# Performance work log

Hardware: AMD Instinct MI355X
Metric: run time of the kernel (lower is better)

The kernel has to match this reference:

```python
import jax, jax.numpy as jnp
import numpy as np

N, NFEAT, NHID, NREL, NCLASS, NHEADS = 4096, 512, 64, 64, 16, 8
ALPHA = 0.2   # LeakyReLU negative slope
NEG = -9e15   # pyGAT mask value


def _gat_layer(x, rel, mask, adj_ad, W, a1, a2, concat):
    # x: [N, Fin], rel: [nrel, Fin], mask: [N, N] bool, adj_ad: [N, nrel]
    xr = x + adj_ad @ rel                 # relation-augmented node features
    h = xr @ W                            # [N, Fout]
    f1 = h @ a1                           # [N]  (a^T[Wh_i||Wh_j] = f1_i + f2_j)
    f2 = h @ a2                           # [N]
    e = jax.nn.leaky_relu(f1[:, None] + f2[None, :], ALPHA)  # [N, N]
    att = jax.nn.softmax(jnp.where(mask, e, NEG), axis=1)
    out = att @ h                         # [N, Fout]
    return jax.nn.elu(out) if concat else out


def setup_inputs() -> dict:
    key = jax.random.key(0)
    ks = jax.random.split(key, 12)
    x = jax.random.normal(ks[0], (N, NFEAT), jnp.float32)
    rel = jax.random.normal(ks[1], (NREL, NFEAT), jnp.float32)
    rel_dict = jax.random.randint(ks[2], (N,), 0, NREL, jnp.int32)
    adj = (jax.random.uniform(ks[3], (N, N)) < 0.01).astype(jnp.float32)
    adj = jnp.maximum(adj, jnp.eye(N, dtype=jnp.float32))  # self loops
    adj_ad = jax.random.uniform(ks[4], (N, NREL), jnp.float32)
    adj_ad = adj_ad / adj_ad.sum(axis=1, keepdims=True)
    s_in = 1.0 / np.sqrt(NFEAT)
    s_hid = 1.0 / np.sqrt(NHID)
    s_cat = 1.0 / np.sqrt(NHID * NHEADS)
    W_heads = jax.random.normal(ks[5], (NHEADS, NFEAT, NHID), jnp.float32) * s_in
    a1_heads = jax.random.normal(ks[6], (NHEADS, NHID), jnp.float32) * s_hid
    a2_heads = jax.random.normal(ks[7], (NHEADS, NHID), jnp.float32) * s_hid
    W_out = jax.random.normal(ks[8], (NHID * NHEADS, NFEAT), jnp.float32) * s_cat
    a1_out = jax.random.normal(ks[9], (NFEAT,), jnp.float32) * s_in
    a2_out = jax.random.normal(ks[10], (NFEAT,), jnp.float32) * s_in
    lin_W = jax.random.normal(ks[11], (NFEAT, NCLASS), jnp.float32) * s_in
    lin_b = jnp.zeros((NCLASS,), jnp.float32)
    return {"x": x, "rel": rel, "rel_dict": rel_dict, "adj": adj, "adj_ad": adj_ad,
            "W_heads": W_heads, "a1_heads": a1_heads, "a2_heads": a2_heads,
            "W_out": W_out, "a1_out": a1_out, "a2_out": a2_out,
            "lin_W": lin_W, "lin_b": lin_b}


def reference(x, rel, rel_dict, adj, adj_ad, W_heads, a1_heads, a2_heads,
              W_out, a1_out, a2_out, lin_W, lin_b):
    # dropout is identity at inference (training=False); rel_dict is only used
    # by the repo to build adj/adj_ad, so it is a non-math constant here.
    mask = adj > 0
    # multi-head GAT layer, heads fused via vmap then concatenated on feature dim
    heads = jax.vmap(lambda W, a1, a2: _gat_layer(x, rel, mask, adj_ad, W, a1, a2, True))(
        W_heads, a1_heads, a2_heads)                      # [H, N, NHID]
    hcat = jnp.moveaxis(heads, 0, 1).reshape(N, NHEADS * NHID)  # [N, H*NHID]
    h2 = _gat_layer(hcat, rel, mask, adj_ad, W_out, a1_out, a2_out, False)  # [N, NFEAT]
    logits = jax.nn.elu(h2 @ lin_W + lin_b)               # [N, NCLASS]
    return jax.nn.log_softmax(logits, axis=1)
```

## Files before the change

kernel.cpp:

```cpp
#include <hip/hip_runtime.h>

#define NN      4096
#define FEAT    512
#define NHID    64
#define NHEADS  8
#define NCLS    16
#define MAXDEG  128
#define ALPHA   0.2f

typedef __bf16 bf16_t;
typedef __bf16 bf16x8_t __attribute__((ext_vector_type(8)));
typedef float  f32x4_t  __attribute__((ext_vector_type(4)));
typedef unsigned short us8_t __attribute__((ext_vector_type(8)));

__device__ inline unsigned short f2bf(float f) {
    unsigned int u = __float_as_uint(f);
    u += 0x7fffu + ((u >> 16) & 1u);
    return (unsigned short)(u >> 16);
}
__device__ inline float bfu2f(unsigned short b) {
    return __uint_as_float(((unsigned int)b) << 16);
}

__global__ __launch_bounds__(256) void prep_kernel(
    const float* __restrict__ adj, int* __restrict__ deg, int* __restrict__ cols,
    const float* __restrict__ adj_ad, const float* __restrict__ rel,
    const float* __restrict__ x, float* __restrict__ R, bf16_t* __restrict__ Abf,
    const float* __restrict__ Wh, const float* __restrict__ Wo,
    unsigned short* __restrict__ WcT, unsigned short* __restrict__ WoT,
    float* __restrict__ f1o, float* __restrict__ f2o) {
    int b = blockIdx.x;
    int t = threadIdx.x;
    __shared__ int wsum[4];
    __shared__ float sa[2][64];
    if (b < NN) {
        const float4* row4 = (const float4*)(adj + (size_t)b * NN);
        float4 v0 = row4[t];
        float4 v1 = row4[t + 256];
        float4 v2 = row4[t + 512];
        float4 v3 = row4[t + 768];
        unsigned mask = 0;
        mask |= (v0.x > 0.0f) << 0;  mask |= (v0.y > 0.0f) << 1;
        mask |= (v0.z > 0.0f) << 2;  mask |= (v0.w > 0.0f) << 3;
        mask |= (v1.x > 0.0f) << 4;  mask |= (v1.y > 0.0f) << 5;
        mask |= (v1.z > 0.0f) << 6;  mask |= (v1.w > 0.0f) << 7;
        mask |= (v2.x > 0.0f) << 8;  mask |= (v2.y > 0.0f) << 9;
        mask |= (v2.z > 0.0f) << 10; mask |= (v2.w > 0.0f) << 11;
        mask |= (v3.x > 0.0f) << 12; mask |= (v3.y > 0.0f) << 13;
        mask |= (v3.z > 0.0f) << 14; mask |= (v3.w > 0.0f) << 15;
        int c = __popc(mask);
        int lane = t & 63;
        int pre = c;
        #pragma unroll
        for (int off = 1; off < 64; off <<= 1) {
            int n = __shfl_up(pre, off);
            if (lane >= off) pre += n;
        }
        if (lane == 63) wsum[t >> 6] = pre;
        __syncthreads();
        int base = pre - c;
        #pragma unroll
        for (int w2 = 0; w2 < 4; ++w2)
            if (w2 < (t >> 6)) base += wsum[w2];
        int* colrow = cols + b * MAXDEG;
        unsigned mm = mask;
        int idx = base;
        while (mm) {
            int bit = __ffs(mm) - 1;
            mm &= mm - 1;
            int j = 4 * t + (bit >> 2) * 1024 + (bit & 3);
            if (idx < MAXDEG) colrow[idx] = j;
            ++idx;
        }
        if (t == 0) {
            int tot = wsum[0] + wsum[1] + wsum[2] + wsum[3];
            deg[b] = tot > MAXDEG ? MAXDEG : tot;
        }
    } else if (b < NN + 2048) {
        int half = t >> 7;
        int tt = t & 127;
        int i = (b - NN) * 2 + half;
        if (tt < 64) sa[half][tt] = adj_ad[i * 64 + tt];
        __syncthreads();
        float4 acc = make_float4(0.f, 0.f, 0.f, 0.f);
        for (int r = 0; r < 64; ++r) {
            float a = sa[half][r];
            float4 rv = ((const float4*)(rel + r * FEAT))[tt];
            acc.x += a * rv.x; acc.y += a * rv.y;
            acc.z += a * rv.z; acc.w += a * rv.w;
        }
        ((float4*)(R + (size_t)i * FEAT))[tt] = acc;
        float4 xv = ((const float4*)(x + (size_t)i * FEAT))[tt];
        ushort4 o;
        o.x = f2bf(acc.x + xv.x); o.y = f2bf(acc.y + xv.y);
        o.z = f2bf(acc.z + xv.z); o.w = f2bf(acc.w + xv.w);
        *(ushort4*)(Abf + (size_t)i * FEAT + 4 * tt) = o;
    } else {
        int gid = (b - NN - 2048) * 256 + t;
        if (gid < 262144) {
            int idx = gid;
            int n = idx >> 9, k = idx & 511;
            int h = n >> 6, f = n & 63;
            WcT[idx] = f2bf(Wh[(h * 512 + k) * 64 + f]);
        } else if (gid < 524288) {
            int idx = gid - 262144;
            int n = idx >> 9, k = idx & 511;
            WoT[idx] = f2bf(Wo[k * 512 + n]);
        } else {
            int idx = gid - 524288;
            ((float4*)f1o)[idx] = make_float4(0.f, 0.f, 0.f, 0.f);
            ((float4*)f2o)[idx] = make_float4(0.f, 0.f, 0.f, 0.f);
        }
    }
}

__global__ __launch_bounds__(256) void gemm_bf16_dot_kernel(
    const bf16_t* __restrict__ A, const bf16_t* __restrict__ Bt,
    unsigned short* __restrict__ Cbf,
    const float* __restrict__ a1, const float* __restrict__ a2,
    float* __restrict__ f1, float* __restrict__ f2, int layer2) {
    __shared__ __align__(16) bf16_t As[64][72];
    __shared__ __align__(16) bf16_t Bs[64][72];
    const int bm = blockIdx.x * 64;
    const int bn = blockIdx.y * 64;
    const int t  = threadIdx.x;
    const int lr = t >> 3;
    const int lc = (t & 7) * 8;
    const int l  = t & 63;
    const int w  = t >> 6;
    const int mrow = w * 16 + (l & 15);
    const int nrow = l & 15;
    const int q8 = (l >> 4) * 8;

    const bf16_t* Ap0 = A  + (size_t)(bm + lr)      * FEAT + lc;
    const bf16_t* Ap1 = A  + (size_t)(bm + 32 + lr) * FEAT + lc;
    const bf16_t* Bp0 = Bt + (size_t)(bn + lr)      * FEAT + lc;
    const bf16_t* Bp1 = Bt + (size_t)(bn + 32 + lr) * FEAT + lc;
    uint4 ra0 = *(const uint4*)(Ap0);
    uint4 ra1 = *(const uint4*)(Ap1);
    uint4 rb0 = *(const uint4*)(Bp0);
    uint4 rb1 = *(const uint4*)(Bp1);

    f32x4_t acc[4] = {};
    for (int k0 = 0; k0 < FEAT; k0 += 64) {
        *(uint4*)&As[lr][lc]      = ra0;
        *(uint4*)&As[32 + lr][lc] = ra1;
        *(uint4*)&Bs[lr][lc]      = rb0;
        *(uint4*)&Bs[32 + lr][lc] = rb1;
        __syncthreads();
        if (k0 + 64 < FEAT) {
            ra0 = *(const uint4*)(Ap0 + k0 + 64);
            ra1 = *(const uint4*)(Ap1 + k0 + 64);
            rb0 = *(const uint4*)(Bp0 + k0 + 64);
            rb1 = *(const uint4*)(Bp1 + k0 + 64);
        }
        #pragma unroll
        for (int kk = 0; kk < 64; kk += 32) {
            bf16x8_t a = *(const bf16x8_t*)&As[mrow][kk + q8];
            #pragma unroll
            for (int nt = 0; nt < 4; ++nt) {
                bf16x8_t b = *(const bf16x8_t*)&Bs[nt * 16 + nrow][kk + q8];
                acc[nt] = __builtin_amdgcn_mfma_f32_16x16x32_bf16(a, b, acc[nt], 0, 0, 0);
            }
        }
        __syncthreads();
    }
    const int crow = bm + w * 16 + (l >> 4) * 4;
    const int ccol = bn + (l & 15);
    #pragma unroll
    for (int nt = 0; nt < 4; ++nt)
        #pragma unroll
        for (int r = 0; r < 4; ++r)
            Cbf[(size_t)(crow + r) * FEAT + ccol + nt * 16] = f2bf(acc[nt][r]);

    float a1v[4], a2v[4];
    #pragma unroll
    for (int nt = 0; nt < 4; ++nt) {
        a1v[nt] = a1[bn + (l & 15) + nt * 16];
        a2v[nt] = a2[bn + (l & 15) + nt * 16];
    }
    float p1[4] = {}, p2[4] = {};
    #pragma unroll
    for (int nt = 0; nt < 4; ++nt)
        #pragma unroll
        for (int r = 0; r < 4; ++r) {
            p1[r] += acc[nt][r] * a1v[nt];
            p2[r] += acc[nt][r] * a2v[nt];
        }
    #pragma unroll
    for (int off = 1; off <= 8; off <<= 1)
        #pragma unroll
        for (int r = 0; r < 4; ++r) {
            p1[r] += __shfl_xor(p1[r], off);
            p2[r] += __shfl_xor(p2[r], off);
        }
    if ((l & 15) == 0) {
        int row = bm + w * 16 + (l >> 4) * 4;
        if (layer2) {
            #pragma unroll
            for (int r = 0; r < 4; ++r) {
                atomicAdd(&f1[row + r], p1[r]);
                atomicAdd(&f2[row + r], p2[r]);
            }
        } else {
            #pragma unroll
            for (int r = 0; r < 4; ++r) {
                f1[blockIdx.y * NN + row + r] = p1[r];
                f2[blockIdx.y * NN + row + r] = p2[r];
            }
        }
    }
}

__global__ __launch_bounds__(512) void att1_kernel(
    const bf16_t* __restrict__ Hbf, const float* __restrict__ f1,
    const float* __restrict__ f2, const int* __restrict__ deg,
    const int* __restrict__ cols, const float* __restrict__ R,
    bf16_t* __restrict__ outbf) {
    int i = blockIdx.x;
    int tid = threadIdx.x;
    int h = tid >> 6;
    int l = tid & 63;
    __shared__ int jl[MAXDEG];
    __shared__ float se[NHEADS][MAXDEG];
    __shared__ float part[NHEADS][FEAT];
    __shared__ float sinv[NHEADS];
    __shared__ int sdeg;
    if (tid == 0) sdeg = deg[i];
    __syncthreads();
    int d = sdeg;
    int dpad = (d + 31) & ~31;
    for (int k = tid; k < dpad; k += 512)
        jl[k] = (k < d) ? cols[i * MAXDEG + k] : i;
    __syncthreads();
    float fi = f1[h * NN + i];
    float lmax = -1e30f;
    for (int k = l; k < d; k += 64) {
        float e = fi + f2[h * NN + jl[k]];
        e = e > 0.0f ? e : ALPHA * e;
        se[h][k] = e;
        lmax = fmaxf(lmax, e);
    }
    for (int off = 32; off; off >>= 1) lmax = fmaxf(lmax, __shfl_down(lmax, off));
    float m = __shfl(lmax, 0);
    float ls = 0.0f;
    for (int k = l; k < d; k += 64) {
        float p = __expf(se[h][k] - m);
        se[h][k] = p;
        ls += p;
    }
    for (int k = d + l; k < dpad; k += 64) se[h][k] = 0.0f;
    for (int off = 32; off; off >>= 1) ls += __shfl_down(ls, off);
    if (l == 0) sinv[h] = 1.0f / ls;
    __syncthreads();
    const int myhead = l >> 3;
    float acc[8] = {};
    for (int k0 = 0; k0 < dpad; k0 += 32) {
        float pw[4];
        const bf16_t* rp[4];
        #pragma unroll
        for (int j = 0; j < 4; ++j) {
            int k = k0 + j * 8 + h;
            pw[j] = se[myhead][k];
            rp[j] = Hbf + (size_t)jl[k] * FEAT + l * 8;
        }
        #pragma unroll
        for (int j = 0; j < 4; ++j) {
            us8_t v = *(const us8_t*)rp[j];
            float p = pw[j];
            #pragma unroll
            for (int q = 0; q < 8; ++q) acc[q] += p * bfu2f(v[q]);
        }
    }
    *(float4*)&part[h][l * 8]     = make_float4(acc[0], acc[1], acc[2], acc[3]);
    *(float4*)&part[h][l * 8 + 4] = make_float4(acc[4], acc[5], acc[6], acc[7]);
    __syncthreads();
    {
        float sum = 0.0f;
        #pragma unroll
        for (int w2 = 0; w2 < NHEADS; ++w2) sum += part[w2][tid];
        float o = sum * sinv[tid >> 6];
        o = o > 0.0f ? o : __expf(o) - 1.0f;
        o += R[(size_t)i * FEAT + tid];
        ((unsigned short*)outbf)[(size_t)i * FEAT + tid] = f2bf(o);
    }
}

__global__ __launch_bounds__(256) void att2_final_kernel(
    const bf16_t* __restrict__ Hbf, const float* __restrict__ f1,
    const float* __restrict__ f2, const int* __restrict__ deg,
    const int* __restrict__ cols, const float* __restrict__ linW,
    const float* __restrict__ linb, float* __restrict__ out) {
    int i = blockIdx.x;
    int t = threadIdx.x;
    __shared__ int jl[MAXDEG];
    __shared__ float sp[MAXDEG];
    __shared__ float red[4];
    __shared__ float part[3][FEAT];
    __shared__ float hrow[FEAT];
    __shared__ float clsred[16][NCLS];
    __shared__ float sl[NCLS];
    __shared__ int sdeg;
    if (t == 0) sdeg = deg[i];
    __syncthreads();
    int d = sdeg;
    int dpad = (d + 15) & ~15;
    if (t < dpad) jl[t] = (t < d) ? cols[i * MAXDEG + t] : i;
    __syncthreads();
    float e = 0.0f, lmax = -1e30f;
    if (t < d) {
        e = f1[i] + f2[jl[t]];
        e = e > 0.0f ? e : ALPHA * e;
        lmax = e;
    }
    for (int off = 32; off; off >>= 1) lmax = fmaxf(lmax, __shfl_down(lmax, off));
    if ((t & 63) == 0) red[t >> 6] = lmax;
    __syncthreads();
    float m = fmaxf(fmaxf(red[0], red[1]), fmaxf(red[2], red[3]));
    float p = 0.0f;
    if (t < d) p = __expf(e - m);
    if (t < dpad) sp[t] = p;
    float ls = p;
    for (int off = 32; off; off >>= 1) ls += __shfl_down(ls, off);
    __syncthreads();
    if ((t & 63) == 0) red[t >> 6] = ls;
    __syncthreads();
    float s = red[0] + red[1] + red[2] + red[3];
    float inv = 1.0f / s;
    const int slot = t >> 6;
    const int cg   = t & 63;
    float acc[8] = {};
    for (int k0 = 0; k0 < dpad; k0 += 16) {
        float pw[4];
        const bf16_t* rp[4];
        #pragma unroll
        for (int j = 0; j < 4; ++j) {
            int k = k0 + j * 4 + slot;
            pw[j] = sp[k];
            rp[j] = Hbf + (size_t)jl[k] * FEAT + cg * 8;
        }
        #pragma unroll
        for (int j = 0; j < 4; ++j) {
            us8_t v = *(const us8_t*)rp[j];
            float pk = pw[j];
            #pragma unroll
            for (int q = 0; q < 8; ++q) acc[q] += pk * bfu2f(v[q]);
        }
    }
    if (slot > 0) {
        float* dst = &part[slot - 1][cg * 8];
        *(float4*)(dst)     = make_float4(acc[0], acc[1], acc[2], acc[3]);
        *(float4*)(dst + 4) = make_float4(acc[4], acc[5], acc[6], acc[7]);
    }
    __syncthreads();
    if (slot == 0) {
        #pragma unroll
        for (int sl2 = 0; sl2 < 3; ++sl2)
            #pragma unroll
            for (int j = 0; j < 8; ++j) acc[j] += part[sl2][cg * 8 + j];
        float* dst = &hrow[cg * 8];
        *(float4*)(dst)     = make_float4(acc[0] * inv, acc[1] * inv, acc[2] * inv, acc[3] * inv);
        *(float4*)(dst + 4) = make_float4(acc[4] * inv, acc[5] * inv, acc[6] * inv, acc[7] * inv);
    }
    __syncthreads();
    {
        int c = t & 15;
        int seg = t >> 4;
        float partial = 0.0f;
        int f0 = seg * 32;
        #pragma unroll 8
        for (int f = f0; f < f0 + 32; ++f) partial += hrow[f] * linW[f * NCLS + c];
        clsred[seg][c] = partial;
    }
    __syncthreads();
    if (t < NCLS) {
        float logit = linb[t];
        #pragma unroll
        for (int seg = 0; seg < 16; ++seg) logit += clsred[seg][t];
        logit = logit > 0.0f ? logit : __expf(logit) - 1.0f;
        sl[t] = logit;
    }
    __syncthreads();
    if (t < NCLS) {
        float mm = sl[0];
        #pragma unroll
        for (int c = 1; c < NCLS; ++c) mm = fmaxf(mm, sl[c]);
        float ssum = 0.0f;
        #pragma unroll
        for (int c = 0; c < NCLS; ++c) ssum += __expf(sl[c] - mm);
        out[i * NCLS + t] = sl[t] - mm - logf(ssum);
    }
}

extern "C" void kernel_launch(void* const* d_in, const int* in_sizes, int n_in,
                              void* d_out, int out_size, void* d_ws, size_t ws_size,
                              hipStream_t stream) {
    const float* x        = (const float*)d_in[0];
    const float* rel      = (const float*)d_in[1];
    const float* adj      = (const float*)d_in[3];
    const float* adj_ad   = (const float*)d_in[4];
    const float* W_heads  = (const float*)d_in[5];
    const float* a1_heads = (const float*)d_in[6];
    const float* a2_heads = (const float*)d_in[7];
    const float* W_out    = (const float*)d_in[8];
    const float* a1_out   = (const float*)d_in[9];
    const float* a2_out   = (const float*)d_in[10];
    const float* lin_W    = (const float*)d_in[11];
    const float* lin_b    = (const float*)d_in[12];
    float* out = (float*)d_out;

    char* ws = (char*)d_ws;
    bf16_t* Abf  = (bf16_t*)(ws);
    bf16_t* Abf2 = (bf16_t*)(ws + (4u  << 20));
    bf16_t* Hbf1 = (bf16_t*)(ws + (8u  << 20));
    bf16_t* Hbf2 = (bf16_t*)(ws + (12u << 20));
    float*  R    = (float*) (ws + (16u << 20));
    bf16_t* WcT  = (bf16_t*)(ws + (24u << 20));
    bf16_t* WoT  = (bf16_t*)(ws + (24u << 20) + (512u << 10));
    float*  f1   = (float*) (ws + (25u << 20));
    float*  f2   = (float*) (ws + (25u << 20) + (128u << 10));
    float*  f1o  = (float*) (ws + (25u << 20) + (256u << 10));
    float*  f2o  = (float*) (ws + (25u << 20) + (272u << 10));
    int*    deg  = (int*)   (ws + (25u << 20) + (288u << 10));
    int*    cols = (int*)   (ws + (26u << 20));

    prep_kernel<<<NN + 2048 + 2052, 256, 0, stream>>>(
        adj, deg, cols, adj_ad, rel, x, R, Abf,
        W_heads, W_out, (unsigned short*)WcT, (unsigned short*)WoT, f1o, f2o);
    gemm_bf16_dot_kernel<<<dim3(64, 8), 256, 0, stream>>>(
        Abf, WcT, (unsigned short*)Hbf1, a1_heads, a2_heads, f1, f2, 0);
    att1_kernel<<<NN, 512, 0, stream>>>(Hbf1, f1, f2, deg, cols, R, Abf2);
    gemm_bf16_dot_kernel<<<dim3(64, 8), 256, 0, stream>>>(
        Abf2, WoT, (unsigned short*)Hbf2, a1_out, a2_out, f1o, f2o, 1);
    att2_final_kernel<<<NN, 256, 0, stream>>>(Hbf2, f1o, f2o, deg, cols, lin_W, lin_b, out);
}
```

Measured before the change: 197.5 us.

## Fold relation term into GEMM K-dimension and overlap adjacency scan with GEMM

Uses (x + adj_ad@rel)@W = [x | adj_ad] @ [W ; rel@W] by widening K from 512 to 576. The prep kernel now writes x and adj_ad in bf16 and computes rel@W rows, which drops the fp32 R buffer and its per-row computation and reads. The adjacency bitmap/column extraction moves from prep into extra blocks of the first GEMM launch so it can overlap with the matmul. The cost is extra GEMM K work, plus rel@W and adj_ad now rounded to bf16, which may change accuracy slightly.

```diff
diff --git a/kernel.cpp b/kernel.cpp
--- a/kernel.cpp
+++ b/kernel.cpp
@@ -2,12 +2,15 @@
 
 #define NN      4096
 #define FEAT    512
+#define KDIM    576
 #define NHID    64
 #define NHEADS  8
 #define NCLS    16
 #define MAXDEG  128
 #define ALPHA   0.2f
 
+#define GEMM_BLKS 512
+
 typedef __bf16 bf16_t;
 typedef __bf16 bf16x8_t __attribute__((ext_vector_type(8)));
 typedef float  f32x4_t  __attribute__((ext_vector_type(4)));
@@ -23,17 +26,83 @@
 }
 
 __global__ __launch_bounds__(256) void prep_kernel(
-    const float* __restrict__ adj, int* __restrict__ deg, int* __restrict__ cols,
     const float* __restrict__ adj_ad, const float* __restrict__ rel,
-    const float* __restrict__ x, float* __restrict__ R, bf16_t* __restrict__ Abf,
+    const float* __restrict__ x, bf16_t* __restrict__ Abf,
+    bf16_t* __restrict__ Abf2,
     const float* __restrict__ Wh, const float* __restrict__ Wo,
     unsigned short* __restrict__ WcT, unsigned short* __restrict__ WoT,
     float* __restrict__ f1o, float* __restrict__ f2o) {
     int b = blockIdx.x;
     int t = threadIdx.x;
-    __shared__ int wsum[4];
-    __shared__ float sa[2][64];
-    if (b < NN) {
+    if (b < 2048) {
+        int half = t >> 7;
+        int tt = t & 127;
+        size_t i = (size_t)b * 2 + half;
+        float4 xv = ((const float4*)(x + i * FEAT))[tt];
+        ushort4 o;
+        o.x = f2bf(xv.x); o.y = f2bf(xv.y);
+        o.z = f2bf(xv.z); o.w = f2bf(xv.w);
+        *(ushort4*)(Abf + i * KDIM + 4 * tt) = o;
+        if (tt < 16) {
+            float4 av = ((const float4*)(adj_ad + i * 64))[tt];
+            ushort4 o2;
+            o2.x = f2bf(av.x); o2.y = f2bf(av.y);
+            o2.z = f2bf(av.z); o2.w = f2bf(av.w);
+            *(ushort4*)(Abf  + i * KDIM + 512 + 4 * tt) = o2;
+            *(ushort4*)(Abf2 + i * KDIM + 512 + 4 * tt) = o2;
+        }
+    } else if (b < 4100) {
+        int gid = (b - 2048) * 256 + t;
+        if (gid < 262144) {
+            int n = gid >> 9, k = gid & 511;
+            int h = n >> 6, f = n & 63;
+            WcT[(size_t)n * KDIM + k] = f2bf(Wh[(h * 512 + k) * 64 + f]);
+        } else if (gid < 524288) {
+            int idx = gid - 262144;
+            int n = idx >> 9, k = idx & 511;
+            WoT[(size_t)n * KDIM + k] = f2bf(Wo[k * 512 + n]);
+        } else {
+            int idx = gid - 524288;
+            ((float4*)f1o)[idx] = make_float4(0.f, 0.f, 0.f, 0.f);
+            ((float4*)f2o)[idx] = make_float4(0.f, 0.f, 0.f, 0.f);
+        }
+    } else {
+        int rb = b - 4100;
+        int r  = rb & 63;
+        int nh = (rb >> 6) & 1;
+        int n  = nh * 256 + t;
+        __shared__ float srow[512];
+        srow[t]       = rel[r * FEAT + t];
+        srow[t + 256] = rel[r * FEAT + 256 + t];
+        __syncthreads();
+        float acc = 0.0f;
+        if (rb < 128) {
+            int h = n >> 6, f = n & 63;
+            const float* p = Wh + (size_t)h * 32768 + f;
+            #pragma unroll 4
+            for (int k = 0; k < 512; ++k) acc += srow[k] * p[(size_t)k * 64];
+            WcT[(size_t)n * KDIM + 512 + r] = f2bf(acc);
+        } else {
+            const float* p = Wo + n;
+            #pragma unroll 4
+            for (int k = 0; k < 512; ++k) acc += srow[k] * p[(size_t)k * 512];
+            WoT[(size_t)n * KDIM + 512 + r] = f2bf(acc);
+        }
+    }
+}
+
+__global__ __launch_bounds__(256) void gemm_bf16_dot_kernel(
+    const bf16_t* __restrict__ A, const bf16_t* __restrict__ Bt,
+    unsigned short* __restrict__ Cbf,
+    const float* __restrict__ a1, const float* __restrict__ a2,
+    float* __restrict__ f1, float* __restrict__ f2, int layer2,
+    const float* __restrict__ adj, int* __restrict__ deg,
+    int* __restrict__ cols) {
+    const int bid = blockIdx.x;
+    const int t   = threadIdx.x;
+    if (bid >= GEMM_BLKS) {
+        int b = bid - GEMM_BLKS;
+        __shared__ int wsum[4];
         const float4* row4 = (const float4*)(adj + (size_t)b * NN);
         float4 v0 = row4[t];
         float4 v1 = row4[t + 256];
@@ -76,54 +145,13 @@
             int tot = wsum[0] + wsum[1] + wsum[2] + wsum[3];
             deg[b] = tot > MAXDEG ? MAXDEG : tot;
         }
-    } else if (b < NN + 2048) {
-        int half = t >> 7;
-        int tt = t & 127;
-        int i = (b - NN) * 2 + half;
-        if (tt < 64) sa[half][tt] = adj_ad[i * 64 + tt];
-        __syncthreads();
-        float4 acc = make_float4(0.f, 0.f, 0.f, 0.f);
-        for (int r = 0; r < 64; ++r) {
-            float a = sa[half][r];
-            float4 rv = ((const float4*)(rel + r * FEAT))[tt];
-            acc.x += a * rv.x; acc.y += a * rv.y;
-            acc.z += a * rv.z; acc.w += a * rv.w;
-        }
-        ((float4*)(R + (size_t)i * FEAT))[tt] = acc;
-        float4 xv = ((const float4*)(x + (size_t)i * FEAT))[tt];
-        ushort4 o;
-        o.x = f2bf(acc.x + xv.x); o.y = f2bf(acc.y + xv.y);
-        o.z = f2bf(acc.z + xv.z); o.w = f2bf(acc.w + xv.w);
-        *(ushort4*)(Abf + (size_t)i * FEAT + 4 * tt) = o;
-    } else {
-        int gid = (b - NN - 2048) * 256 + t;
-        if (gid < 262144) {
-            int idx = gid;
-            int n = idx >> 9, k = idx & 511;
-            int h = n >> 6, f = n & 63;
-            WcT[idx] = f2bf(Wh[(h * 512 + k) * 64 + f]);
-        } else if (gid < 524288) {
-            int idx = gid - 262144;
-            int n = idx >> 9, k = idx & 511;
-            WoT[idx] = f2bf(Wo[k * 512 + n]);
-        } else {
-            int idx = gid - 524288;
-            ((float4*)f1o)[idx] = make_float4(0.f, 0.f, 0.f, 0.f);
-            ((float4*)f2o)[idx] = make_float4(0.f, 0.f, 0.f, 0.f);
-        }
-    }
-}
-
-__global__ __launch_bounds__(256) void gemm_bf16_dot_kernel(
-    const bf16_t* __restrict__ A, const bf16_t* __restrict__ Bt,
-    unsigned short* __restrict__ Cbf,
-    const float* __restrict__ a1, const float* __restrict__ a2,
-    float* __restrict__ f1, float* __restrict__ f2, int layer2) {
+        return;
+    }
     __shared__ __align__(16) bf16_t As[64][72];
     __shared__ __align__(16) bf16_t Bs[64][72];
-    const int bm = blockIdx.x * 64;
-    const int bn = blockIdx.y * 64;
-    const int t  = threadIdx.x;
+    const int bm = (bid & 63) * 64;
+    const int by = bid >> 6;
+    const int bn = by * 64;
     const int lr = t >> 3;
     const int lc = (t & 7) * 8;
     const int l  = t & 63;
@@ -132,23 +160,23 @@
     const int nrow = l & 15;
     const int q8 = (l >> 4) * 8;
 
-    const bf16_t* Ap0 = A  + (size_t)(bm + lr)      * FEAT + lc;
-    const bf16_t* Ap1 = A  + (size_t)(bm + 32 + lr) * FEAT + lc;
-    const bf16_t* Bp0 = Bt + (size_t)(bn + lr)      * FEAT + lc;
-    const bf16_t* Bp1 = Bt + (size_t)(bn + 32 + lr) * FEAT + lc;
+    const bf16_t* Ap0 = A  + (size_t)(bm + lr)      * KDIM + lc;
+    const bf16_t* Ap1 = A  + (size_t)(bm + 32 + lr) * KDIM + lc;
+    const bf16_t* Bp0 = Bt + (size_t)(bn + lr)      * KDIM + lc;
+    const bf16_t* Bp1 = Bt + (size_t)(bn + 32 + lr) * KDIM + lc;
     uint4 ra0 = *(const uint4*)(Ap0);
     uint4 ra1 = *(const uint4*)(Ap1);
     uint4 rb0 = *(const uint4*)(Bp0);
     uint4 rb1 = *(const uint4*)(Bp1);
 
     f32x4_t acc[4] = {};
-    for (int k0 = 0; k0 < FEAT; k0 += 64) {
+    for (int k0 = 0; k0 < KDIM; k0 += 64) {
         *(uint4*)&As[lr][lc]      = ra0;
         *(uint4*)&As[32 + lr][lc] = ra1;
         *(uint4*)&Bs[lr][lc]      = rb0;
         *(uint4*)&Bs[32 + lr][lc] = rb1;
         __syncthreads();
-        if (k0 + 64 < FEAT) {
+        if (k0 + 64 < KDIM) {
             ra0 = *(const uint4*)(Ap0 + k0 + 64);
             ra1 = *(const uint4*)(Ap1 + k0 + 64);
             rb0 = *(const uint4*)(Bp0 + k0 + 64);
@@ -205,8 +233,8 @@
         } else {
             #pragma unroll
             for (int r = 0; r < 4; ++r) {
-                f1[blockIdx.y * NN + row + r] = p1[r];
-                f2[blockIdx.y * NN + row + r] = p2[r];
+                f1[by * NN + row + r] = p1[r];
+                f2[by * NN + row + r] = p2[r];
             }
         }
     }
@@ -215,8 +243,7 @@
 __global__ __launch_bounds__(512) void att1_kernel(
     const bf16_t* __restrict__ Hbf, const float* __restrict__ f1,
     const float* __restrict__ f2, const int* __restrict__ deg,
-    const int* __restrict__ cols, const float* __restrict__ R,
-    bf16_t* __restrict__ outbf) {
+    const int* __restrict__ cols, bf16_t* __restrict__ outbf) {
     int i = blockIdx.x;
     int tid = threadIdx.x;
     int h = tid >> 6;
@@ -281,8 +308,7 @@
         for (int w2 = 0; w2 < NHEADS; ++w2) sum += part[w2][tid];
         float o = sum * sinv[tid >> 6];
         o = o > 0.0f ? o : __expf(o) - 1.0f;
-        o += R[(size_t)i * FEAT + tid];
-        ((unsigned short*)outbf)[(size_t)i * FEAT + tid] = f2bf(o);
+        ((unsigned short*)outbf)[(size_t)i * KDIM + tid] = f2bf(o);
     }
 }
 
@@ -411,26 +437,27 @@
 
     char* ws = (char*)d_ws;
     bf16_t* Abf  = (bf16_t*)(ws);
-    bf16_t* Abf2 = (bf16_t*)(ws + (4u  << 20));
-    bf16_t* Hbf1 = (bf16_t*)(ws + (8u  << 20));
-    bf16_t* Hbf2 = (bf16_t*)(ws + (12u << 20));
-    float*  R    = (float*) (ws + (16u << 20));
-    bf16_t* WcT  = (bf16_t*)(ws + (24u << 20));
-    bf16_t* WoT  = (bf16_t*)(ws + (24u << 20) + (512u << 10));
-    float*  f1   = (float*) (ws + (25u << 20));
-    float*  f2   = (float*) (ws + (25u << 20) + (128u << 10));
-    float*  f1o  = (float*) (ws + (25u << 20) + (256u << 10));
-    float*  f2o  = (float*) (ws + (25u << 20) + (272u << 10));
-    int*    deg  = (int*)   (ws + (25u << 20) + (288u << 10));
-    int*    cols = (int*)   (ws + (26u << 20));
-
-    prep_kernel<<<NN + 2048 + 2052, 256, 0, stream>>>(
-        adj, deg, cols, adj_ad, rel, x, R, Abf,
-        W_heads, W_out, (unsigned short*)WcT, (unsigned short*)WoT, f1o, f2o);
-    gemm_bf16_dot_kernel<<<dim3(64, 8), 256, 0, stream>>>(
-        Abf, WcT, (unsigned short*)Hbf1, a1_heads, a2_heads, f1, f2, 0);
-    att1_kernel<<<NN, 512, 0, stream>>>(Hbf1, f1, f2, deg, cols, R, Abf2);
-    gemm_bf16_dot_kernel<<<dim3(64, 8), 256, 0, stream>>>(
-        Abf2, WoT, (unsigned short*)Hbf2, a1_out, a2_out, f1o, f2o, 1);
+    bf16_t* Abf2 = (bf16_t*)(ws + (5u  << 20));
+    bf16_t* Hbf1 = (bf16_t*)(ws + (10u << 20));
+    bf16_t* Hbf2 = (bf16_t*)(ws + (14u << 20));
+    bf16_t* WcT  = (bf16_t*)(ws + (18u << 20));
+    bf16_t* WoT  = (bf16_t*)(ws + (19u << 20));
+    float*  f1   = (float*) (ws + (20u << 20));
+    float*  f2   = (float*) (ws + (20u << 20) + (128u << 10));
+    float*  f1o  = (float*) (ws + (20u << 20) + (256u << 10));
+    float*  f2o  = (float*) (ws + (20u << 20) + (272u << 10));
+    int*    deg  = (int*)   (ws + (20u << 20) + (288u << 10));
+    int*    cols = (int*)   (ws + (21u << 20));
+
+    prep_kernel<<<4356, 256, 0, stream>>>(
+        adj_ad, rel, x, Abf, Abf2, W_heads, W_out,
+        (unsigned short*)WcT, (unsigned short*)WoT, f1o, f2o);
+    gemm_bf16_dot_kernel<<<GEMM_BLKS + NN, 256, 0, stream>>>(
+        Abf, WcT, (unsigned short*)Hbf1, a1_heads, a2_heads, f1, f2, 0,
+        adj, deg, cols);
+    att1_kernel<<<NN, 512, 0, stream>>>(Hbf1, f1, f2, deg, cols, Abf2);
+    gemm_bf16_dot_kernel<<<GEMM_BLKS, 256, 0, stream>>>(
+        Abf2, WoT, (unsigned short*)Hbf2, a1_out, a2_out, f1o, f2o, 1,
+        nullptr, nullptr, nullptr);
     att2_final_kernel<<<NN, 256, 0, stream>>>(Hbf2, f1o, f2o, deg, cols, lin_W, lin_b, out);
 }
```

After: 206.2 us. 1.04x slower.
